# Performance work log

Measured on AMD Instinct MI355X. Metric: run time of the kernel, lower is better.

The kernel has to match this reference:

```python
import jax, jax.numpy as jnp
import numpy as np

N = 50000
E = 800000
D = 128   # input_dim
O = 128   # output_dim


def setup_inputs() -> dict:
    key = jax.random.key(0)
    ks = jax.random.split(key, 12)
    s = 0.05
    inp = {
        "x": jax.random.normal(ks[0], (N, D), dtype=jnp.float32),
        "edge_index": jax.random.randint(ks[1], (2, E), 0, N, dtype=jnp.int64),
        # lin_src_to_dst / lin_dst_to_src
        "w_s2d": jax.random.normal(ks[2], (D, O), dtype=jnp.float32) * s,
        "b_s2d": jnp.zeros((O,), dtype=jnp.float32),
        "w_d2s": jax.random.normal(ks[3], (D, O), dtype=jnp.float32) * s,
        "b_d2s": jnp.zeros((O,), dtype=jnp.float32),
        # edge_mlp: Linear(2D -> D), ReLU, Linear(D -> 1)
        "w_e1": jax.random.normal(ks[4], (2 * D, D), dtype=jnp.float32) * s,
        "b_e1": jnp.zeros((D,), dtype=jnp.float32),
        "w_e2": jax.random.normal(ks[5], (D, 1), dtype=jnp.float32) * s,
        "b_e2": jnp.zeros((1,), dtype=jnp.float32),
        # gate_mlp: Linear(2O -> O), ReLU, Linear(O -> 1)
        "w_g1": jax.random.normal(ks[6], (2 * O, O), dtype=jnp.float32) * s,
        "b_g1": jnp.zeros((O,), dtype=jnp.float32),
        "w_g2": jax.random.normal(ks[7], (O, 1), dtype=jnp.float32) * s,
        "b_g2": jnp.zeros((1,), dtype=jnp.float32),
    }
    return inp


def reference(x, edge_index, w_s2d, b_s2d, w_d2s, b_d2s,
              w_e1, b_e1, w_e2, b_e2, w_g1, b_g1, w_g2, b_g2):
    num_nodes = x.shape[0]
    src = edge_index[0]
    dst = edge_index[1]

    x_src = x[src]                      # [E, D]
    x_dst = x[dst]                      # [E, D]

    # edge-wise contribution score a_ij in (0,1)
    edge_input = jnp.concatenate([x_src, x_dst], axis=-1)          # [E, 2D]
    h_e = jax.nn.relu(edge_input @ w_e1 + b_e1)                    # [E, D]
    edge_score = jax.nn.sigmoid((h_e @ w_e2 + b_e2)[:, 0])         # [E]

    # directional messages, scaled by edge score
    msg_in = (x_src @ w_s2d + b_s2d) * edge_score[:, None]         # [E, O]
    msg_out = (x_dst @ w_d2s + b_d2s) * edge_score[:, None]        # [E, O]

    # scatter-add to nodes
    h_in = jax.ops.segment_sum(msg_in, dst, num_segments=num_nodes)   # [N, O]
    h_out = jax.ops.segment_sum(msg_out, src, num_segments=num_nodes) # [N, O]

    # degree normalization (clamped at 1)
    ones = jnp.ones((src.shape[0],), dtype=x.dtype)
    in_deg = jnp.maximum(jax.ops.segment_sum(ones, dst, num_segments=num_nodes), 1.0)
    out_deg = jnp.maximum(jax.ops.segment_sum(ones, src, num_segments=num_nodes), 1.0)
    h_in = h_in / in_deg[:, None]
    h_out = h_out / out_deg[:, None]

    # node-wise gate fusing the two directions
    gate_input = jnp.concatenate([h_in, h_out], axis=-1)           # [N, 2O]
    h_g = jax.nn.relu(gate_input @ w_g1 + b_g1)                    # [N, O]
    g = jax.nn.sigmoid(h_g @ w_g2 + b_g2)                          # [N, 1]

    fused = g * h_in + (1.0 - g) * h_out                           # [N, O]
    # input_dim == output_dim -> residual is Identity
    return fused + x
```

## Files before the change

### kernel.cpp

```cpp
#include <hip/hip_runtime.h>

#define N_NODES 50000
#define N_EDGES 800000
#define NBKT 391
#define BKT 128
#define MAXREC 2560
#define EPB 4096

typedef unsigned int u32;
typedef unsigned short u16;
typedef __attribute__((ext_vector_type(2))) float float2v;
typedef __attribute__((ext_vector_type(8))) short bf16x8;
typedef __attribute__((ext_vector_type(4))) float f32x4;

__device__ __forceinline__ float bf_lo(u32 v){ return __uint_as_float(v << 16); }
__device__ __forceinline__ float bf_hi(u32 v){ return __uint_as_float(v & 0xffff0000u); }
__device__ __forceinline__ u16 f2bf(float f){
    u32 u = __float_as_uint(f);
    u += 0x7fffu + ((u >> 16) & 1u);
    return (u16)(u >> 16);
}

#if __has_builtin(__builtin_amdgcn_cvt_pk_f32_fp8) && __has_builtin(__builtin_amdgcn_cvt_pk_fp8_f32)
#define HW_FP8 1
#else
#define HW_FP8 0
#endif

__device__ __forceinline__ u32 enc1_e4m3(float f){
    u32 u = __float_as_uint(f);
    u32 s = (u >> 24) & 0x80u;
    u32 a = u & 0x7fffffffu;
    if (a >= 0x43e00000u) return s | 0x7eu;
    if (a < 0x3c800000u){
        float af = __uint_as_float(a) * 512.f;
        u32 m = (u32)(af + 0.5f);
        return s | m;
    }
    int e = (int)(a >> 23) - 127;
    u32 mant = (a >> 20) & 7u;
    u32 rnd = (a >> 19) & 1u;
    u32 sticky = (a & 0x7ffffu) ? 1u : 0u;
    u32 code = ((u32)(e + 7) << 3) | mant;
    code += (rnd & (sticky | (mant & 1u)));
    if (code > 0x7eu) code = 0x7eu;
    return s | code;
}

template<bool HI>
__device__ __forceinline__ float2v dec2_word(u32 v){
#if HW_FP8
    return __builtin_amdgcn_cvt_pk_f32_fp8(v, HI);
#else
    u32 v16 = HI ? (v >> 16) : (v & 0xffffu);
    float2v r;
    #pragma unroll
    for (int t = 0; t < 2; t++){
        u32 b = (v16 >> (8 * t)) & 0xffu;
        u32 e = (b >> 3) & 15u, m = b & 7u;
        float fv = e ? __uint_as_float(((e + 120u) << 23) | (m << 20)) : (float)m * 0.001953125f;
        r[t] = (b & 0x80u) ? -fv : fv;
    }
    return r;
#endif
}
__device__ __forceinline__ u32 encpk_lo(float a, float b, u32 old){
#if HW_FP8
    return (u32)__builtin_amdgcn_cvt_pk_fp8_f32(a, b, (int)old, false);
#else
    return (old & 0xffff0000u) | enc1_e4m3(a) | (enc1_e4m3(b) << 8);
#endif
}
__device__ __forceinline__ u32 encpk_hi(float a, float b, u32 old){
#if HW_FP8
    return (u32)__builtin_amdgcn_cvt_pk_fp8_f32(a, b, (int)old, true);
#else
    return (old & 0x0000ffffu) | (enc1_e4m3(a) << 16) | (enc1_e4m3(b) << 24);
#endif
}

__global__ void zero_bcnt_kernel(u32* __restrict__ bcnt){
    int i = threadIdx.x;
    if (i < 2 * NBKT) bcnt[i] = 0u;
}

__global__ void prep_kernel(const float* __restrict__ w_s2d, const float* __restrict__ w_d2s,
                            const float* __restrict__ w_e1, const float* __restrict__ w_g1,
                            const float* __restrict__ b_e1,
                            u16* __restrict__ pk1, u16* __restrict__ pkM,
                            u16* __restrict__ pkG, float* __restrict__ bias1){
    int idx = blockIdx.x * 256 + threadIdx.x;
    if (idx < 32768){
        int j = idx & 7, g = (idx >> 3) & 3, ch = (idx >> 5) & 255, ks = idx >> 13;
        int k = ks * 32 + g * 8 + j;
        float v = (ch < 128) ? w_e1[k * 128 + ch] : w_e1[(128 + k) * 128 + (ch - 128)];
        pk1[idx] = f2bf(v);
    } else if (idx < 65536){
        int i2 = idx - 32768;
        int j = i2 & 7, g = (i2 >> 3) & 3, ch = (i2 >> 5) & 255, ks = i2 >> 13;
        int k = ks * 32 + g * 8 + j;
        float v = (ch < 128) ? w_s2d[k * 128 + ch] : w_d2s[k * 128 + (ch - 128)];
        pkM[i2] = f2bf(v);
    } else if (idx < 98304){
        int i2 = idx - 65536;
        int j = i2 & 7, g = (i2 >> 3) & 3, oc = (i2 >> 5) & 127, ks = i2 >> 12;
        int k = ks * 32 + g * 8 + j;
        pkG[i2] = f2bf(w_g1[k * 128 + oc]);
    } else if (idx < 98560){
        int o = idx - 98304;
        bias1[o] = (o < 128) ? b_e1[o] : 0.f;
    }
}

__global__ void xcast_kernel(const float* __restrict__ x, u32* __restrict__ xb){
    int i = blockIdx.x * 256 + threadIdx.x;
    if (i < N_NODES * 64){
        float2 v = ((const float2*)x)[i];
        xb[i] = (u32)f2bf(v.x) | ((u32)f2bf(v.y) << 16);
    }
}

__global__ __launch_bounds__(256) void proj_mfma_kernel(const u16* __restrict__ xb16,
        const u16* __restrict__ pk1, const float* __restrict__ bias1, u32* __restrict__ T1){
    const int tid = threadIdx.x;
    const int w = tid >> 6, l = tid & 63;
    const int l16 = l & 15, lg = l >> 4;
    const int n0 = blockIdx.x * 16;
    const int node = n0 + l16;
    bf16x8 bx[4];
    #pragma unroll
    for (int ks = 0; ks < 4; ks++)
        bx[ks] = *(const bf16x8*)(xb16 + node * 128 + ks * 32 + lg * 8);
    #pragma unroll
    for (int ct = 0; ct < 4; ct++){
        const int ch0 = w * 64 + ct * 16;
        f32x4 acc = {0.f, 0.f, 0.f, 0.f};
        #pragma unroll
        for (int ks = 0; ks < 4; ks++){
            bf16x8 a = *(const bf16x8*)(pk1 + ((ks * 256 + ch0 + l16) * 4 + lg) * 8);
            acc = __builtin_amdgcn_mfma_f32_16x16x32_bf16(a, bx[ks], acc, 0, 0, 0);
        }
        const int chb = ch0 + lg * 4;
        float f0 = acc[0] + bias1[chb],     f1 = acc[1] + bias1[chb + 1];
        float f2 = acc[2] + bias1[chb + 2], f3 = acc[3] + bias1[chb + 3];
        u32 wd = encpk_lo(f0, f1, 0u);
        wd = encpk_hi(f2, f3, wd);
        T1[node * 64 + (chb >> 2)] = wd;
    }
}

__global__ __launch_bounds__(256) void edge_score_kernel(const u32* __restrict__ T1w, const int* __restrict__ eidx,
        const float* __restrict__ w_e2, const float* __restrict__ b_e2,
        u16* __restrict__ score){
    const int l16 = threadIdx.x & 15;
    const int e = blockIdx.x * 16 + (threadIdx.x >> 4);
    const int src = eidx[e];
    const int dst = eidx[N_EDGES + e];
    const uint2 a8 = *(const uint2*)(T1w + src * 64 + l16 * 2);
    const uint2 b8 = *(const uint2*)(T1w + dst * 64 + 32 + l16 * 2);
    float2v a0 = dec2_word<false>(a8.x), a1 = dec2_word<true>(a8.x);
    float2v a2 = dec2_word<false>(a8.y), a3 = dec2_word<true>(a8.y);
    float2v b0 = dec2_word<false>(b8.x), b1 = dec2_word<true>(b8.x);
    float2v b2 = dec2_word<false>(b8.y), b3 = dec2_word<true>(b8.y);
    const float4 w0 = ((const float4*)w_e2)[l16 * 2];
    const float4 w1 = ((const float4*)w_e2)[l16 * 2 + 1];
    float p = fmaxf(a0[0] + b0[0], 0.f) * w0.x + fmaxf(a0[1] + b0[1], 0.f) * w0.y
            + fmaxf(a1[0] + b1[0], 0.f) * w0.z + fmaxf(a1[1] + b1[1], 0.f) * w0.w
            + fmaxf(a2[0] + b2[0], 0.f) * w1.x + fmaxf(a2[1] + b2[1], 0.f) * w1.y
            + fmaxf(a3[0] + b3[0], 0.f) * w1.z + fmaxf(a3[1] + b3[1], 0.f) * w1.w;
    p += __shfl_xor(p, 1, 64);
    p += __shfl_xor(p, 2, 64);
    p += __shfl_xor(p, 4, 64);
    p += __shfl_xor(p, 8, 64);
    if (l16 == 0){
        float sc = 1.f / (1.f + __expf(-(p + b_e2[0])));
        score[e] = f2bf(sc);
    }
}

__global__ __launch_bounds__(256) void count_kernel(const int* __restrict__ eidx, u32* __restrict__ bcnt){
    __shared__ u32 h[2 * NBKT];
    const int tid = threadIdx.x;
    for (int i = tid; i < 2 * NBKT; i += 256) h[i] = 0u;
    __syncthreads();
    const int e0 = blockIdx.x * EPB;
    for (int i = tid; i < EPB; i += 256){
        int e = e0 + i;
        if (e < N_EDGES){
            atomicAdd(&h[eidx[N_EDGES + e] >> 7], 1u);
            atomicAdd(&h[NBKT + (eidx[e] >> 7)], 1u);
        }
    }
    __syncthreads();
    for (int i = tid; i < 2 * NBKT; i += 256){
        u32 v = h[i];
        if (v) atomicAdd(&bcnt[i], v);
    }
}

__global__ __launch_bounds__(512) void bucket_scan_kernel(const u32* __restrict__ bcnt,
        u32* __restrict__ bbase, u32* __restrict__ bnext){
    __shared__ u32 sa[512], sb[512];
    const int t = threadIdx.x;
    const u32* c = bcnt + blockIdx.x * NBKT;
    u32* base = bbase + blockIdx.x * (NBKT + 1);
    u32* nxt  = bnext + blockIdx.x * NBKT;
    sa[t] = (t < NBKT) ? c[t] : 0u;
    __syncthreads();
    u32 *a = sa, *b = sb;
    for (int off = 1; off < 512; off <<= 1){
        u32 v = a[t]; if (t >= off) v += a[t - off];
        b[t] = v; __syncthreads();
        u32* tmp = a; a = b; b = tmp;
    }
    if (t < NBKT){
        u32 ex = t ? a[t - 1] : 0u;
        base[t] = ex; nxt[t] = ex;
        if (t == NBKT - 1) base[NBKT] = a[t];
    }
}

__global__ __launch_bounds__(256) void bucket1_kernel(const int* __restrict__ eidx, const u16* __restrict__ score,
        u32* __restrict__ bnext, uint2* __restrict__ Bd, uint2* __restrict__ Bs){
    __shared__ u32 hd[NBKT], hs[NBKT];
    __shared__ u32 rbd[NBKT], rbs[NBKT];
    __shared__ u32 ld[NBKT], ls[NBKT];
    const int tid = threadIdx.x;
    for (int i = tid; i < NBKT; i += 256){ hd[i] = 0u; hs[i] = 0u; ld[i] = 0u; ls[i] = 0u; }
    __syncthreads();
    const int e0 = blockIdx.x * EPB;
    for (int i = tid; i < EPB; i += 256){
        int e = e0 + i;
        if (e < N_EDGES){
            atomicAdd(&hd[eidx[N_EDGES + e] >> 7], 1u);
            atomicAdd(&hs[eidx[e] >> 7], 1u);
        }
    }
    __syncthreads();
    for (int i = tid; i < NBKT; i += 256){
        rbd[i] = hd[i] ? atomicAdd(&bnext[i], hd[i]) : 0u;
        rbs[i] = hs[i] ? atomicAdd(&bnext[NBKT + i], hs[i]) : 0u;
    }
    __syncthreads();
    for (int i = tid; i < EPB; i += 256){
        int e = e0 + i;
        if (e < N_EDGES){
            int src = eidx[e], dst = eidx[N_EDGES + e];
            u32 sc = (u32)score[e] << 16;
            int bd = dst >> 7;
            u32 r = atomicAdd(&ld[bd], 1u);
            Bd[rbd[bd] + r] = make_uint2(sc | (u32)src, (u32)(dst & 127));
            int bs_ = src >> 7;
            u32 r2 = atomicAdd(&ls[bs_], 1u);
            Bs[rbs[bs_] + r2] = make_uint2(sc | (u32)dst, (u32)(src & 127));
        }
    }
}

__global__ __launch_bounds__(256) void bucket2_kernel(const uint2* __restrict__ Bd, const uint2* __restrict__ Bs,
        const u32* __restrict__ bbase,
        u32* __restrict__ cnt_dst, u32* __restrict__ start_dst,
        u32* __restrict__ cnt_src, u32* __restrict__ start_src,
        u32* __restrict__ in_pay, u32* __restrict__ out_pay){
    __shared__ u32 pays[MAXREC];
    __shared__ u16 locs[MAXREC];
    __shared__ u32 hist[BKT], nxt[BKT], pref[BKT];
    const int tid = threadIdx.x;
    const int side = blockIdx.x >= NBKT ? 1 : 0;
    const int b = side ? blockIdx.x - NBKT : blockIdx.x;
    const uint2* __restrict__ B = side ? Bs : Bd;
    const u32* bb = bbase + side * (NBKT + 1);
    const u32 base = bb[b];
    const u32 nrec = bb[b + 1] - base;
    u32* cnto = side ? cnt_src : cnt_dst;
    u32* sto  = side ? start_src : start_dst;
    u32* payo = side ? out_pay : in_pay;
    for (int i = tid; i < BKT; i += 256) hist[i] = 0u;
    __syncthreads();
    for (u32 i = tid; i < nrec; i += 256){
        uint2 r = B[base + i];
        if (i < MAXREC){ pays[i] = r.x; locs[i] = (u16)r.y; }
        atomicAdd(&hist[r.y & (BKT - 1)], 1u);
    }
    __syncthreads();
    if (tid < BKT) pref[tid] = hist[tid];
    __syncthreads();
    for (int off = 1; off < BKT; off <<= 1){
        u32 v = 0;
        if (tid < BKT){ v = pref[tid]; if (tid >= off) v += pref[tid - off]; }
        __syncthreads();
        if (tid < BKT) pref[tid] = v;
        __syncthreads();
    }
    if (tid < BKT){
        u32 ex = tid ? pref[tid - 1] : 0u;
        u32 gstart = base + ex;
        nxt[tid] = gstart;
        int node = b * BKT + tid;
        if (node < N_NODES){ cnto[node] = hist[tid]; sto[node] = gstart; }
    }
    __syncthreads();
    for (u32 i = tid; i < nrec; i += 256){
        u32 pay; int loc;
        if (i < MAXREC){ pay = pays[i]; loc = locs[i]; }
        else { uint2 r = B[base + i]; pay = r.x; loc = (int)(r.y & (BKT - 1)); }
        u32 pos = atomicAdd(&nxt[loc], 1u);
        payo[pos] = pay;
    }
}

__global__ __launch_bounds__(256) void gather_kernel(const u32* __restrict__ xb,
        const u32* __restrict__ in_pay, const u32* __restrict__ out_pay,
        const u32* __restrict__ cnt_dst, const u32* __restrict__ start_dst,
        const u32* __restrict__ cnt_src, const u32* __restrict__ start_src,
        u32* __restrict__ Y, float* __restrict__ ssin, float* __restrict__ ssout){
    const int w = threadIdx.x >> 6, lane = threadIdx.x & 63;
    const int node = blockIdx.x * 2 + (w >> 1);
    const int dir = w & 1;
    const u32* __restrict__ pay = dir ? out_pay : in_pay;
    const u32 deg = dir ? cnt_src[node] : cnt_dst[node];
    const u32 st  = dir ? start_src[node] : start_dst[node];
    const uint2* __restrict__ xb2 = (const uint2*)xb;
    const int half = lane >> 5, l5 = lane & 31;
    float a0 = 0.f, a1 = 0.f, a2 = 0.f, a3 = 0.f, ss = 0.f;
    u32 j = (u32)half;
    for (; j + 6 < deg; j += 8){
        u32 p0 = pay[st+j], p1 = pay[st+j+2], p2 = pay[st+j+4], p3 = pay[st+j+6];
        uint2 v0 = xb2[(p0 & 0xffffu)*32 + l5], v1 = xb2[(p1 & 0xffffu)*32 + l5];
        uint2 v2 = xb2[(p2 & 0xffffu)*32 + l5], v3 = xb2[(p3 & 0xffffu)*32 + l5];
        float s0 = __uint_as_float(p0 & 0xffff0000u), s1 = __uint_as_float(p1 & 0xffff0000u);
        float s2 = __uint_as_float(p2 & 0xffff0000u), s3 = __uint_as_float(p3 & 0xffff0000u);
        a0 += s0*bf_lo(v0.x) + s1*bf_lo(v1.x) + s2*bf_lo(v2.x) + s3*bf_lo(v3.x);
        a1 += s0*bf_hi(v0.x) + s1*bf_hi(v1.x) + s2*bf_hi(v2.x) + s3*bf_hi(v3.x);
        a2 += s0*bf_lo(v0.y) + s1*bf_lo(v1.y) + s2*bf_lo(v2.y) + s3*bf_lo(v3.y);
        a3 += s0*bf_hi(v0.y) + s1*bf_hi(v1.y) + s2*bf_hi(v2.y) + s3*bf_hi(v3.y);
        ss += s0 + s1 + s2 + s3;
    }
    for (; j < deg; j += 2){
        u32 pl = pay[st + j];
        uint2 v = xb2[(pl & 0xffffu)*32 + l5];
        float sc = __uint_as_float(pl & 0xffff0000u);
        a0 += sc * bf_lo(v.x); a1 += sc * bf_hi(v.x);
        a2 += sc * bf_lo(v.y); a3 += sc * bf_hi(v.y);
        ss += sc;
    }
    a0 += __shfl_xor(a0, 32, 64);
    a1 += __shfl_xor(a1, 32, 64);
    a2 += __shfl_xor(a2, 32, 64);
    a3 += __shfl_xor(a3, 32, 64);
    ss += __shfl_xor(ss, 32, 64);
    if (half == 0){
        uint2 o;
        o.x = (u32)f2bf(a0) | ((u32)f2bf(a1) << 16);
        o.y = (u32)f2bf(a2) | ((u32)f2bf(a3) << 16);
        *(uint2*)(Y + node * 128 + dir * 64 + l5 * 2) = o;
    }
    if (lane == 0){
        if (dir) ssout[node] = ss; else ssin[node] = ss;
    }
}

__global__ __launch_bounds__(256) void finale_mfma_kernel(const u32* __restrict__ Yw,
        const float* __restrict__ x,
        const u16* __restrict__ pkM, const u16* __restrict__ pkG,
        const float* __restrict__ b_s2d, const float* __restrict__ b_d2s,
        const float* __restrict__ ssin, const float* __restrict__ ssout,
        const u32* __restrict__ cnt_dst, const u32* __restrict__ cnt_src,
        const float* __restrict__ b_g1, const float* __restrict__ w_g2, const float* __restrict__ b_g2,
        float* __restrict__ out){
    __shared__ u32 Hsh[16][132];
    __shared__ float part[16][17];
    __shared__ float gl[16];
    const int tid = threadIdx.x;
    const int w = tid >> 6, l = tid & 63;
    const int l16 = l & 15, lg = l >> 4;
    const int n0 = blockIdx.x * 16;
    const int node = n0 + l16;
    const int dir = w >> 1;
    const int cb = (w & 1) * 64;
    const u16* Yh = (const u16*)Yw;
    bf16x8 yf[4];
    #pragma unroll
    for (int ks = 0; ks < 4; ks++)
        yf[ks] = *(const bf16x8*)(Yh + node * 256 + dir * 128 + ks * 32 + lg * 8);
    const float ssv  = dir ? ssout[node] : ssin[node];
    const float dinv = 1.f / fmaxf((float)(dir ? cnt_src[node] : cnt_dst[node]), 1.f);
    const float* bv = dir ? b_d2s : b_s2d;
    #pragma unroll
    for (int ct = 0; ct < 4; ct++){
        const int chl = cb + ct * 16;
        f32x4 acc = {0.f, 0.f, 0.f, 0.f};
        #pragma unroll
        for (int ks = 0; ks < 4; ks++){
            bf16x8 a = *(const bf16x8*)(pkM + ((ks * 256 + dir * 128 + chl + l16) * 4 + lg) * 8);
            acc = __builtin_amdgcn_mfma_f32_16x16x32_bf16(a, yf[ks], acc, 0, 0, 0);
        }
        const int chb = chl + lg * 4;
        float h0 = (acc[0] + ssv * bv[chb])     * dinv;
        float h1 = (acc[1] + ssv * bv[chb + 1]) * dinv;
        float h2 = (acc[2] + ssv * bv[chb + 2]) * dinv;
        float h3 = (acc[3] + ssv * bv[chb + 3]) * dinv;
        const int wi = (dir * 128 + chb) >> 1;
        Hsh[l16][wi]     = (u32)f2bf(h0) | ((u32)f2bf(h1) << 16);
        Hsh[l16][wi + 1] = (u32)f2bf(h2) | ((u32)f2bf(h3) << 16);
    }
    __syncthreads();
    bf16x8 hb[8];
    #pragma unroll
    for (int ks = 0; ks < 8; ks++)
        hb[ks] = *(const bf16x8*)((const u16*)&Hsh[l16][0] + ks * 32 + lg * 8);
    float p = 0.f;
    #pragma unroll
    for (int ct2 = 0; ct2 < 2; ct2++){
        const int oc0 = w * 32 + ct2 * 16;
        f32x4 acc = {0.f, 0.f, 0.f, 0.f};
        #pragma unroll
        for (int ks = 0; ks < 8; ks++){
            bf16x8 a = *(const bf16x8*)(pkG + ((ks * 128 + oc0 + l16) * 4 + lg) * 8);
            acc = __builtin_amdgcn_mfma_f32_16x16x32_bf16(a, hb[ks], acc, 0, 0, 0);
        }
        const int ob = oc0 + lg * 4;
        #pragma unroll
        for (int r = 0; r < 4; r++)
            p += fmaxf(acc[r] + b_g1[ob + r], 0.f) * w_g2[ob + r];
    }
    part[l16][w * 4 + lg] = p;
    __syncthreads();
    if (tid < 16){
        float s = 0.f;
        #pragma unroll
        for (int i = 0; i < 16; i++) s += part[tid][i];
        gl[tid] = 1.f / (1.f + __expf(-(s + b_g2[0])));
    }
    __syncthreads();
    {
        const int nn = tid >> 4, o = (tid & 15) * 8;
        const float gv = gl[nn];
        const int gbase = (n0 + nn) * 128 + o;
        float4 x0 = *(const float4*)(x + gbase);
        float4 x1 = *(const float4*)(x + gbase + 4);
        float r[8];
        #pragma unroll
        for (int t = 0; t < 4; t++){
            u32 hi = Hsh[nn][(o >> 1) + t];
            u32 ho = Hsh[nn][64 + (o >> 1) + t];
            r[2*t]   = gv * bf_lo(hi) + (1.f - gv) * bf_lo(ho);
            r[2*t+1] = gv * bf_hi(hi) + (1.f - gv) * bf_hi(ho);
        }
        *(float4*)(out + gbase)     = make_float4(r[0]+x0.x, r[1]+x0.y, r[2]+x0.z, r[3]+x0.w);
        *(float4*)(out + gbase + 4) = make_float4(r[4]+x1.x, r[5]+x1.y, r[6]+x1.z, r[7]+x1.w);
    }
}

extern "C" void kernel_launch(void* const* d_in, const int* in_sizes, int n_in,
                              void* d_out, int out_size, void* d_ws, size_t ws_size,
                              hipStream_t stream){
    const float* x     = (const float*)d_in[0];
    const int*   ei    = (const int*)d_in[1];
    const float* w_s2d = (const float*)d_in[2];
    const float* b_s2d = (const float*)d_in[3];
    const float* w_d2s = (const float*)d_in[4];
    const float* b_d2s = (const float*)d_in[5];
    const float* w_e1  = (const float*)d_in[6];
    const float* b_e1  = (const float*)d_in[7];
    const float* w_e2  = (const float*)d_in[8];
    const float* b_e2  = (const float*)d_in[9];
    const float* w_g1  = (const float*)d_in[10];
    const float* b_g1  = (const float*)d_in[11];
    const float* w_g2  = (const float*)d_in[12];
    const float* b_g2  = (const float*)d_in[13];
    float* out = (float*)d_out;
    u32*   T1  = (u32*)d_out;
    uint2* Bd  = (uint2*)d_out;
    uint2* Bs  = Bd + N_EDGES;
    u32*   Y   = (u32*)d_out;

    char* ws = (char*)d_ws;
    size_t off = 0;
    #define TAKE(name, bytes) char* name = ws + off; off += (((size_t)(bytes)) + 511) & ~(size_t)511;
    TAKE(pk1_b,   32768 * 2)
    TAKE(pkM_b,   32768 * 2)
    TAKE(pkG_b,   32768 * 2)
    TAKE(bias1_b, 256 * 4)
    TAKE(xb_b,    (size_t)N_NODES * 128 * 2)
    TAKE(score_b, (size_t)N_EDGES * 2)
    TAKE(bcnt_b,  (size_t)2 * NBKT * 4)
    TAKE(bbase_b, (size_t)2 * (NBKT + 1) * 4)
    TAKE(bnext_b, (size_t)2 * NBKT * 4)
    TAKE(cnt_b,   (size_t)2 * N_NODES * 4)
    TAKE(sd_b,    (size_t)N_NODES * 4)
    TAKE(ss2_b,   (size_t)N_NODES * 4)
    TAKE(ipay_b,  (size_t)N_EDGES * 4)
    TAKE(opay_b,  (size_t)N_EDGES * 4)
    TAKE(ssin_b,  (size_t)N_NODES * 4)
    TAKE(ssout_b, (size_t)N_NODES * 4)
    #undef TAKE
    (void)ws_size; (void)in_sizes; (void)n_in; (void)out_size;

    zero_bcnt_kernel<<<1, 1024, 0, stream>>>((u32*)bcnt_b);
    prep_kernel<<<(98560 + 255) / 256, 256, 0, stream>>>(w_s2d, w_d2s, w_e1, w_g1, b_e1,
        (u16*)pk1_b, (u16*)pkM_b, (u16*)pkG_b, (float*)bias1_b);
    xcast_kernel<<<(N_NODES * 64 + 255) / 256, 256, 0, stream>>>(x, (u32*)xb_b);
    count_kernel<<<(N_EDGES + EPB - 1) / EPB, 256, 0, stream>>>(ei, (u32*)bcnt_b);
    proj_mfma_kernel<<<N_NODES / 16, 256, 0, stream>>>((const u16*)xb_b,
        (const u16*)pk1_b, (const float*)bias1_b, T1);
    edge_score_kernel<<<N_EDGES / 16, 256, 0, stream>>>((const u32*)T1, ei, w_e2, b_e2,
        (u16*)score_b);
    bucket_scan_kernel<<<2, 512, 0, stream>>>((const u32*)bcnt_b, (u32*)bbase_b, (u32*)bnext_b);
    bucket1_kernel<<<(N_EDGES + EPB - 1) / EPB, 256, 0, stream>>>(ei, (const u16*)score_b,
        (u32*)bnext_b, Bd, Bs);
    bucket2_kernel<<<2 * NBKT, 256, 0, stream>>>(Bd, Bs, (const u32*)bbase_b,
        (u32*)cnt_b, (u32*)sd_b, (u32*)cnt_b + N_NODES, (u32*)ss2_b,
        (u32*)ipay_b, (u32*)opay_b);
    gather_kernel<<<N_NODES / 2, 256, 0, stream>>>((const u32*)xb_b,
        (const u32*)ipay_b, (const u32*)opay_b,
        (const u32*)cnt_b, (const u32*)sd_b, (const u32*)cnt_b + N_NODES, (const u32*)ss2_b,
        Y, (float*)ssin_b, (float*)ssout_b);
    finale_mfma_kernel<<<N_NODES / 16, 256, 0, stream>>>((const u32*)Y, x,
        (const u16*)pkM_b, (const u16*)pkG_b, b_s2d, b_d2s,
        (const float*)ssin_b, (const float*)ssout_b,
        (const u32*)cnt_b, (const u32*)cnt_b + N_NODES,
        b_g1, w_g2, b_g2, out);
}
```

Measured before the change: 238.4 us.

## Gather node features in FP8 and merge setup kernels into one launch

The gather stage now reads node features from a new FP8 (e4m3) copy of x instead of the bf16 copy, halving the bytes fetched per neighbour in the random-access gather. The FP8 copy is produced alongside the bf16 cast in a single setup kernel that also absorbs the weight-packing and bucket-counter zeroing kernels, removing two launches. The cost is lower precision in the aggregated messages, plus an extra FP8 write of x during setup.

```diff
diff --git a/kernel.cpp b/kernel.cpp
--- a/kernel.cpp
+++ b/kernel.cpp
@@ -6,6 +6,7 @@
 #define BKT 128
 #define MAXREC 2560
 #define EPB 4096
+#define XCBLK 6250
 
 typedef unsigned int u32;
 typedef unsigned short u16;
@@ -79,44 +80,47 @@
 #endif
 }
 
-__global__ void zero_bcnt_kernel(u32* __restrict__ bcnt){
-    int i = threadIdx.x;
-    if (i < 2 * NBKT) bcnt[i] = 0u;
-}
-
-__global__ void prep_kernel(const float* __restrict__ w_s2d, const float* __restrict__ w_d2s,
-                            const float* __restrict__ w_e1, const float* __restrict__ w_g1,
-                            const float* __restrict__ b_e1,
-                            u16* __restrict__ pk1, u16* __restrict__ pkM,
-                            u16* __restrict__ pkG, float* __restrict__ bias1){
-    int idx = blockIdx.x * 256 + threadIdx.x;
-    if (idx < 32768){
-        int j = idx & 7, g = (idx >> 3) & 3, ch = (idx >> 5) & 255, ks = idx >> 13;
-        int k = ks * 32 + g * 8 + j;
-        float v = (ch < 128) ? w_e1[k * 128 + ch] : w_e1[(128 + k) * 128 + (ch - 128)];
-        pk1[idx] = f2bf(v);
-    } else if (idx < 65536){
-        int i2 = idx - 32768;
-        int j = i2 & 7, g = (i2 >> 3) & 3, ch = (i2 >> 5) & 255, ks = i2 >> 13;
-        int k = ks * 32 + g * 8 + j;
-        float v = (ch < 128) ? w_s2d[k * 128 + ch] : w_d2s[k * 128 + (ch - 128)];
-        pkM[i2] = f2bf(v);
-    } else if (idx < 98304){
-        int i2 = idx - 65536;
-        int j = i2 & 7, g = (i2 >> 3) & 3, oc = (i2 >> 5) & 127, ks = i2 >> 12;
-        int k = ks * 32 + g * 8 + j;
-        pkG[i2] = f2bf(w_g1[k * 128 + oc]);
-    } else if (idx < 98560){
-        int o = idx - 98304;
-        bias1[o] = (o < 128) ? b_e1[o] : 0.f;
-    }
-}
-
-__global__ void xcast_kernel(const float* __restrict__ x, u32* __restrict__ xb){
-    int i = blockIdx.x * 256 + threadIdx.x;
-    if (i < N_NODES * 64){
-        float2 v = ((const float2*)x)[i];
-        xb[i] = (u32)f2bf(v.x) | ((u32)f2bf(v.y) << 16);
+__global__ __launch_bounds__(256) void setup_kernel(const float* __restrict__ x,
+        const float* __restrict__ w_s2d, const float* __restrict__ w_d2s,
+        const float* __restrict__ w_e1, const float* __restrict__ w_g1,
+        const float* __restrict__ b_e1,
+        uint2* __restrict__ xb2, u32* __restrict__ xf8,
+        u16* __restrict__ pk1, u16* __restrict__ pkM,
+        u16* __restrict__ pkG, float* __restrict__ bias1, u32* __restrict__ bcnt){
+    const int blk = blockIdx.x, tid = threadIdx.x;
+    if (blk < XCBLK){
+        int i = blk * 256 + tid;
+        float4 v = ((const float4*)x)[i];
+        uint2 o;
+        o.x = (u32)f2bf(v.x) | ((u32)f2bf(v.y) << 16);
+        o.y = (u32)f2bf(v.z) | ((u32)f2bf(v.w) << 16);
+        xb2[i] = o;
+        u32 w8 = encpk_lo(v.x, v.y, 0u);
+        xf8[i] = encpk_hi(v.z, v.w, w8);
+    } else if (blk < XCBLK + 386){
+        int idx = (blk - XCBLK) * 256 + tid;
+        if (idx < 32768){
+            int j = idx & 7, g = (idx >> 3) & 3, ch = (idx >> 5) & 255, ks = idx >> 13;
+            int k = ks * 32 + g * 8 + j;
+            float v = (ch < 128) ? w_e1[k * 128 + ch] : w_e1[(128 + k) * 128 + (ch - 128)];
+            pk1[idx] = f2bf(v);
+        } else if (idx < 65536){
+            int i2 = idx - 32768;
+            int j = i2 & 7, g = (i2 >> 3) & 3, ch = (i2 >> 5) & 255, ks = i2 >> 13;
+            int k = ks * 32 + g * 8 + j;
+            float v = (ch < 128) ? w_s2d[k * 128 + ch] : w_d2s[k * 128 + (ch - 128)];
+            pkM[i2] = f2bf(v);
+        } else if (idx < 98304){
+            int i2 = idx - 65536;
+            int j = i2 & 7, g = (i2 >> 3) & 3, oc = (i2 >> 5) & 127, ks = i2 >> 12;
+            int k = ks * 32 + g * 8 + j;
+            pkG[i2] = f2bf(w_g1[k * 128 + oc]);
+        } else if (idx < 98560){
+            int o = idx - 98304;
+            bias1[o] = (o < 128) ? b_e1[o] : 0.f;
+        }
+    } else {
+        for (int i = tid; i < 2 * NBKT; i += 256) bcnt[i] = 0u;
     }
 }
 
@@ -309,7 +313,7 @@
     }
 }
 
-__global__ __launch_bounds__(256) void gather_kernel(const u32* __restrict__ xb,
+__global__ __launch_bounds__(256) void gather_kernel(const u32* __restrict__ xf8,
         const u32* __restrict__ in_pay, const u32* __restrict__ out_pay,
         const u32* __restrict__ cnt_dst, const u32* __restrict__ start_dst,
         const u32* __restrict__ cnt_src, const u32* __restrict__ start_src,
@@ -320,28 +324,32 @@
     const u32* __restrict__ pay = dir ? out_pay : in_pay;
     const u32 deg = dir ? cnt_src[node] : cnt_dst[node];
     const u32 st  = dir ? start_src[node] : start_dst[node];
-    const uint2* __restrict__ xb2 = (const uint2*)xb;
     const int half = lane >> 5, l5 = lane & 31;
     float a0 = 0.f, a1 = 0.f, a2 = 0.f, a3 = 0.f, ss = 0.f;
     u32 j = (u32)half;
     for (; j + 6 < deg; j += 8){
         u32 p0 = pay[st+j], p1 = pay[st+j+2], p2 = pay[st+j+4], p3 = pay[st+j+6];
-        uint2 v0 = xb2[(p0 & 0xffffu)*32 + l5], v1 = xb2[(p1 & 0xffffu)*32 + l5];
-        uint2 v2 = xb2[(p2 & 0xffffu)*32 + l5], v3 = xb2[(p3 & 0xffffu)*32 + l5];
+        u32 v0 = xf8[(p0 & 0xffffu)*32 + l5], v1 = xf8[(p1 & 0xffffu)*32 + l5];
+        u32 v2 = xf8[(p2 & 0xffffu)*32 + l5], v3 = xf8[(p3 & 0xffffu)*32 + l5];
         float s0 = __uint_as_float(p0 & 0xffff0000u), s1 = __uint_as_float(p1 & 0xffff0000u);
         float s2 = __uint_as_float(p2 & 0xffff0000u), s3 = __uint_as_float(p3 & 0xffff0000u);
-        a0 += s0*bf_lo(v0.x) + s1*bf_lo(v1.x) + s2*bf_lo(v2.x) + s3*bf_lo(v3.x);
-        a1 += s0*bf_hi(v0.x) + s1*bf_hi(v1.x) + s2*bf_hi(v2.x) + s3*bf_hi(v3.x);
-        a2 += s0*bf_lo(v0.y) + s1*bf_lo(v1.y) + s2*bf_lo(v2.y) + s3*bf_lo(v3.y);
-        a3 += s0*bf_hi(v0.y) + s1*bf_hi(v1.y) + s2*bf_hi(v2.y) + s3*bf_hi(v3.y);
+        float2v e0l = dec2_word<false>(v0), e0h = dec2_word<true>(v0);
+        float2v e1l = dec2_word<false>(v1), e1h = dec2_word<true>(v1);
+        float2v e2l = dec2_word<false>(v2), e2h = dec2_word<true>(v2);
+        float2v e3l = dec2_word<false>(v3), e3h = dec2_word<true>(v3);
+        a0 += s0*e0l[0] + s1*e1l[0] + s2*e2l[0] + s3*e3l[0];
+        a1 += s0*e0l[1] + s1*e1l[1] + s2*e2l[1] + s3*e3l[1];
+        a2 += s0*e0h[0] + s1*e1h[0] + s2*e2h[0] + s3*e3h[0];
+        a3 += s0*e0h[1] + s1*e1h[1] + s2*e2h[1] + s3*e3h[1];
         ss += s0 + s1 + s2 + s3;
     }
     for (; j < deg; j += 2){
         u32 pl = pay[st + j];
-        uint2 v = xb2[(pl & 0xffffu)*32 + l5];
+        u32 v = xf8[(pl & 0xffffu)*32 + l5];
         float sc = __uint_as_float(pl & 0xffff0000u);
-        a0 += sc * bf_lo(v.x); a1 += sc * bf_hi(v.x);
-        a2 += sc * bf_lo(v.y); a3 += sc * bf_hi(v.y);
+        float2v el = dec2_word<false>(v), eh = dec2_word<true>(v);
+        a0 += sc * el[0]; a1 += sc * el[1];
+        a2 += sc * eh[0]; a3 += sc * eh[1];
         ss += sc;
     }
     a0 += __shfl_xor(a0, 32, 64);
@@ -483,6 +491,7 @@
     TAKE(pkG_b,   32768 * 2)
     TAKE(bias1_b, 256 * 4)
     TAKE(xb_b,    (size_t)N_NODES * 128 * 2)
+    TAKE(xf8_b,   (size_t)N_NODES * 128)
     TAKE(score_b, (size_t)N_EDGES * 2)
     TAKE(bcnt_b,  (size_t)2 * NBKT * 4)
     TAKE(bbase_b, (size_t)2 * (NBKT + 1) * 4)
@@ -497,10 +506,9 @@
     #undef TAKE
     (void)ws_size; (void)in_sizes; (void)n_in; (void)out_size;
 
-    zero_bcnt_kernel<<<1, 1024, 0, stream>>>((u32*)bcnt_b);
-    prep_kernel<<<(98560 + 255) / 256, 256, 0, stream>>>(w_s2d, w_d2s, w_e1, w_g1, b_e1,
-        (u16*)pk1_b, (u16*)pkM_b, (u16*)pkG_b, (float*)bias1_b);
-    xcast_kernel<<<(N_NODES * 64 + 255) / 256, 256, 0, stream>>>(x, (u32*)xb_b);
+    setup_kernel<<<XCBLK + 386 + 1, 256, 0, stream>>>(x, w_s2d, w_d2s, w_e1, w_g1, b_e1,
+        (uint2*)xb_b, (u32*)xf8_b, (u16*)pk1_b, (u16*)pkM_b, (u16*)pkG_b,
+        (float*)bias1_b, (u32*)bcnt_b);
     count_kernel<<<(N_EDGES + EPB - 1) / EPB, 256, 0, stream>>>(ei, (u32*)bcnt_b);
     proj_mfma_kernel<<<N_NODES / 16, 256, 0, stream>>>((const u16*)xb_b,
         (const u16*)pk1_b, (const float*)bias1_b, T1);
@@ -512,7 +520,7 @@
     bucket2_kernel<<<2 * NBKT, 256, 0, stream>>>(Bd, Bs, (const u32*)bbase_b,
         (u32*)cnt_b, (u32*)sd_b, (u32*)cnt_b + N_NODES, (u32*)ss2_b,
         (u32*)ipay_b, (u32*)opay_b);
-    gather_kernel<<<N_NODES / 2, 256, 0, stream>>>((const u32*)xb_b,
+    gather_kernel<<<N_NODES / 2, 256, 0, stream>>>((const u32*)xf8_b,
         (const u32*)ipay_b, (const u32*)opay_b,
         (const u32*)cnt_b, (const u32*)sd_b, (const u32*)cnt_b + N_NODES, (const u32*)ss2_b,
         Y, (float*)ssin_b, (float*)ssout_b);
```

New measurement: 224.2 us. -5.9%, faster.
